# Kernel tuning notes

Hardware: AMD Instinct MI355X
Metric: run time of the kernel (lower is better)

Reference implementation:

```python
import jax, jax.numpy as jnp
import numpy as np
import math

DIM = 1024      # dim == dim_attn (required by value-reshape)
HEAD = 16
KV = 128        # K_v routing slots
HD = DIM // HEAD
N = 50000       # number of nodes


def setup_inputs() -> dict:
    key = jax.random.key(0)
    ks = jax.random.split(key, 8)
    s = lambda fan_in: 1.0 / np.sqrt(fan_in)
    return {
        "x": jax.random.normal(ks[0], (N, DIM), jnp.float32),
        "node_index": jax.random.normal(ks[1], (N, 4), jnp.float32),
        # nn.Linear(dim, dim_attn)
        "Wq": jax.random.normal(ks[2], (DIM, DIM), jnp.float32) * s(DIM),
        "bq": jnp.zeros((DIM,), jnp.float32),
        # nn.Parameter key (K_v, head, head_dim), torch.randn init
        "key_p": jax.random.normal(ks[3], (KV, HEAD, HD), jnp.float32),
        # nn.Linear(dim, dim)
        "Wv": jax.random.normal(ks[4], (DIM, DIM), jnp.float32) * s(DIM),
        "bv": jnp.zeros((DIM,), jnp.float32),
        # gate params, shape (head, 1)
        "alpha": jnp.full((HEAD, 1), math.log(9.0), jnp.float32),
        "beta": jnp.full((HEAD, 1), math.log(0.01), jnp.float32),
        # nn.Linear(4, head*K_v)
        "Wb": jax.random.normal(ks[5], (HEAD * KV, 4), jnp.float32) * s(4),
        "bb": jnp.zeros((HEAD * KV,), jnp.float32),
    }


def _mh_sinkhorn(A, num_iters=3, eps=0.05):
    # A: (N, H, K). Faithful to the per-head torch sinkhorn (Q transposed to
    # (K, N)): row sums are over the node axis, col sums over the slot axis.
    n = A.shape[0]
    k = A.shape[2]
    Q = jnp.exp(A / eps)
    Q = Q / jnp.sum(Q, axis=(0, 2), keepdims=True)          # total-sum norm per head
    for _ in range(num_iters):
        Q = Q / jnp.sum(Q, axis=0, keepdims=True) / k       # rows of Q.T (per slot)
        Q = Q / jnp.sum(Q, axis=2, keepdims=True) / n       # cols of Q.T (per node)
    return Q * n


def reference(x, node_index, Wq, bq, key_p, Wv, bv, alpha, beta, Wb, bb):
    n = x.shape[0]
    q = (x @ Wq.T + bq).reshape(n, HEAD, HD)
    attn = jnp.einsum('nhd,rhd->nhr', q, key_p) / np.float32(np.sqrt(HD))
    bias = (node_index @ Wb.T + bb).reshape(n, HEAD, KV)
    attn = attn + bias                                       # (n, H, K_v)
    xv = (x @ Wv.T + bv).reshape(n, HEAD, HD)
    v = jnp.einsum('nhr,nhd->rhd', jax.nn.sigmoid(attn), xv)  # (K_v, H, D)
    cons = _mh_sinkhorn(jax.nn.softmax(attn, axis=-1))
    v = jnp.einsum('nhr,rhd->nhd', cons, v)
    out = jax.nn.sigmoid(alpha) * xv + jax.nn.sigmoid(beta) * v  # (H,1) broadcasts
    return out.reshape(n, DIM)
```

## Files before the change

### kernel.cpp

```cpp
#include <hip/hip_runtime.h>

#define N_NODES 50000
#define MPAD    50176
#define DIM     1024
#define HEAD    16
#define KV      128
#define HD      64
#define NGRP    98

typedef unsigned short ushort_t;
typedef short short8 __attribute__((ext_vector_type(8)));
typedef float f32x4 __attribute__((ext_vector_type(4)));

__device__ inline unsigned short f2bf(float f){
  union { float f; unsigned u; } v; v.f = f;
  unsigned u = v.u;
  unsigned r = (u + 0x7FFFu + ((u >> 16) & 1u)) >> 16;
  return (unsigned short)r;
}
__device__ inline float bf2f(unsigned short u){
  union { unsigned u; float f; } v; v.u = ((unsigned)u) << 16; return v.f;
}

__device__ inline void gload_lds16(const void* g, void* l){
  __builtin_amdgcn_global_load_lds(
      (const __attribute__((address_space(1))) void*)g,
      (__attribute__((address_space(3))) void*)l, 16, 0, 0);
}

__device__ inline short8 frag64(const ushort_t* lds, int row, int kk, int lane){
  int c  = kk*4 + (lane >> 4);
  int cc = c ^ (row & 7);
  return *(const short8*)(lds + row*64 + cc*8);
}
__device__ inline short8 frag128(const ushort_t* lds, int row, int kk, int lane){
  int c  = kk*4 + (lane >> 4);
  int cc = c ^ (row & 7);
  return *(const short8*)(lds + row*128 + cc*8);
}

__global__ void k_zero(float* p, int n){
  int i = blockIdx.x*256 + threadIdx.x;
  if (i < n) p[i] = 0.f;
}

__global__ void k_prep_x(const float* __restrict__ x, ushort_t* __restrict__ x_bf){
  int idx = blockIdx.x*256 + threadIdx.x;
  int row = idx >> 7, c = idx & 127;
  const float4* s = (const float4*)(x + (size_t)row*1024 + c*8);
  float4 f0 = s[0], f1 = s[1];
  short8 v;
  v[0]=(short)f2bf(f0.x); v[1]=(short)f2bf(f0.y); v[2]=(short)f2bf(f0.z); v[3]=(short)f2bf(f0.w);
  v[4]=(short)f2bf(f1.x); v[5]=(short)f2bf(f1.y); v[6]=(short)f2bf(f1.z); v[7]=(short)f2bf(f1.w);
  int sc = (c & ~7) | ((c ^ row) & 7);
  *(short8*)(x_bf + (size_t)row*1024 + sc*8) = v;
}

__global__ void k_prep_w(const float* __restrict__ Wq, const float* __restrict__ Wv,
                         ushort_t* __restrict__ w_bf){
  int idx = blockIdx.x*256 + threadIdx.x;
  int j = idx >> 10, k = idx & 1023;
  float v = (j < 1024) ? Wq[idx] : Wv[(size_t)(j-1024)*1024 + k];
  int d = k & 63;
  int scol = (k & ~63) | ((((d>>3) ^ (j & 7)) & 7) << 3) | (d & 7);
  w_bf[(size_t)j*1024 + scol] = f2bf(v);
}

__global__ void k_prep_key(const float* __restrict__ key_p, ushort_t* __restrict__ key_bf){
  int idx = blockIdx.x*256 + threadIdx.x;
  int h = idx >> 13, rem = idx & 8191;
  int r = rem >> 6, d = rem & 63;
  float v = key_p[(size_t)(r*HEAD + h)*HD + d];
  int pos = ((((d>>3) ^ (r & 7)) & 7) << 3) | (d & 7);
  key_bf[(size_t)h*8192 + r*64 + pos] = f2bf(v);
}

__global__ void k_vreduce(const float* __restrict__ vp, float* __restrict__ vout){
  int i = blockIdx.x*256 + threadIdx.x;
  float s = 0.f;
  for (int gg = 0; gg < NGRP; ++gg) s += vp[(size_t)gg*131072 + i];
  vout[i] = s;
}

__global__ __launch_bounds__(512) void k_gemm(const ushort_t* __restrict__ x_bf,
    const ushort_t* __restrict__ w_bf, const float* __restrict__ bq,
    const float* __restrict__ bv, ushort_t* __restrict__ q_bf, float* xv_out){
  extern __shared__ char gsm[];
  ushort_t* As = (ushort_t*)gsm;
  ushort_t* Bs = (ushort_t*)(gsm + 65536);
  const int tid = threadIdx.x, lane = tid & 63;
  const int wid = tid >> 6, wr = wid >> 2, wc = wid & 3;
  int b = blockIdx.x;
  int wg = (b & 7)*196 + (b >> 3);
  const int bm0 = (wg >> 3) * 256, bn0 = (wg & 7) * 256;

  f32x4 acc[8][4];
  #pragma unroll
  for (int m=0;m<8;m++)
    #pragma unroll
    for (int n=0;n<4;n++) acc[m][n] = (f32x4){0.f,0.f,0.f,0.f};

  const ushort_t* asrc = x_bf + (size_t)bm0*1024;
  const ushort_t* bsrc = w_bf + (size_t)bn0*1024;

#define STAGE(kt, bi)                                                    \
  { _Pragma("unroll")                                                    \
    for (int it=0; it<4; ++it){                                          \
      int chunk = it*512 + tid;                                          \
      int r = chunk >> 3, c = chunk & 7;                                 \
      gload_lds16(asrc + (size_t)r*1024 + (kt)*64 + c*8,                 \
                  As + (bi)*16384 + chunk*8);                            \
    }                                                                    \
    _Pragma("unroll")                                                    \
    for (int it=0; it<4; ++it){                                          \
      int chunk = it*512 + tid;                                          \
      int r = chunk >> 3, c = chunk & 7;                                 \
      gload_lds16(bsrc + (size_t)r*1024 + (kt)*64 + c*8,                 \
                  Bs + (bi)*16384 + chunk*8);                            \
    }                                                                    \
  }

  STAGE(0, 0);
  STAGE(1, 1);

  for (int kt = 0; kt < 16; ++kt){
    const int cur = kt & 1;
    if (kt == 15) { asm volatile("s_waitcnt vmcnt(0)" ::: "memory"); }
    else          { asm volatile("s_waitcnt vmcnt(8)" ::: "memory"); }
    __builtin_amdgcn_s_barrier();

    const ushort_t* ab  = As + cur*16384;
    const ushort_t* bb_ = Bs + cur*16384;
    #pragma unroll
    for (int kk=0;kk<2;kk++){
      short8 bfr[4];
      #pragma unroll
      for (int n=0;n<4;n++) bfr[n] = frag64(bb_, wc*64 + n*16 + (lane&15), kk, lane);
      #pragma unroll
      for (int m=0;m<8;m++){
        short8 af = frag64(ab, wr*128 + m*16 + (lane&15), kk, lane);
        #pragma unroll
        for (int n=0;n<4;n++)
          acc[m][n] = __builtin_amdgcn_mfma_f32_16x16x32_bf16(af, bfr[n], acc[m][n], 0,0,0);
      }
    }
    __builtin_amdgcn_s_barrier();
    if (kt + 2 < 16) STAGE(kt+2, cur);
  }
#undef STAGE

  const bool isq = bn0 < 1024;
  #pragma unroll
  for (int n=0;n<4;n++){
    int col = bn0 + wc*64 + n*16 + (lane & 15);
    float bias = isq ? bq[col] : bv[col - 1024];
    #pragma unroll
    for (int m=0;m<8;m++){
      #pragma unroll
      for (int j=0;j<4;j++){
        int row = bm0 + wr*128 + m*16 + (lane>>4)*4 + j;
        float val = acc[m][n][j] + bias;
        if (isq){
          int d = col & 63;
          int scol = (col & ~63) | ((((d>>3) ^ (row & 7)) & 7) << 3) | (d & 7);
          q_bf[(size_t)row*1024 + scol] = f2bf(val);
        } else if (row < N_NODES){
          xv_out[(size_t)row*1024 + (col - 1024)] = val;
        }
      }
    }
  }
}

template<int PHASE>
__global__ __launch_bounds__(256) void k_attn(
    const ushort_t* __restrict__ q_bf, const ushort_t* __restrict__ key_bf,
    const float* __restrict__ node_index, const float* __restrict__ Wb,
    const float* __restrict__ bb, const float* __restrict__ colsum_in,
    float* __restrict__ colsum_out, const float* __restrict__ v_fin,
    float* __restrict__ v_part, float* xv_out,
    const float* __restrict__ alpha, const float* __restrict__ beta)
{
  constexpr int QB    = (PHASE == 2) ? 1 : 2;
  constexpr int O_Q   = 0;
  constexpr int O_KEY = O_Q + QB*8192;
  constexpr int O_NI  = O_KEY + 16384;
  constexpr int O_WB  = O_NI + QB*1024;
  constexpr int O_RED = O_WB + 2560;
  constexpr int O_COL = O_RED + 2048;
  constexpr int O_W   = O_COL + 512;
  constexpr int O_X1  = O_W + 512;
  constexpr int O_X2  = O_X1 + 16384;

  extern __shared__ char smem[];
  ushort_t* q_lds   = (ushort_t*)(smem + O_Q);
  ushort_t* key_lds = (ushort_t*)(smem + O_KEY);
  float* ni_lds  = (float*)(smem + O_NI);
  float* wb_lds  = (float*)(smem + O_WB);
  float* red_lds = (float*)(smem + O_RED);
  float* col_acc = (float*)(smem + O_COL);
  float* w_lds   = (float*)(smem + O_W);
  ushort_t* sigT     = (ushort_t*)(smem + O_X1);
  ushort_t* xvT      = (ushort_t*)(smem + O_X2);
  ushort_t* vT       = (ushort_t*)(smem + O_X1);
  ushort_t* cons_lds = (ushort_t*)(smem + O_X2);
  float*    out_lds  = (float*)(smem + O_X2);

  const int tid = threadIdx.x, lane = tid & 63, wid = tid >> 6;
  const int h    = blockIdx.x & 15;
  const int g    = blockIdx.x >> 4;
  const int base = g * 512;
  int NT = (MPAD - base) >> 6; if (NT > 8) NT = 8;

  #pragma unroll
  for (int it = 0; it < 4; ++it){
    int chunk = it*256 + tid;
    gload_lds16(key_bf + (size_t)h*8192 + chunk*8, key_lds + chunk*8);
  }
  #pragma unroll
  for (int it = 0; it < 2; ++it){
    int chunk = it*256 + tid;
    int r = chunk >> 3, c = chunk & 7;
    gload_lds16(q_bf + (size_t)(base + r)*1024 + h*64 + c*8, q_lds + chunk*8);
  }
  { int r = tid >> 2, c = tid & 3;
    ni_lds[tid] = (base + r < N_NODES) ? node_index[(size_t)(base + r)*4 + c] : 0.f; }
  if (tid < 128){
    #pragma unroll
    for (int c=0;c<4;c++) wb_lds[tid*5+c] = Wb[(size_t)(h*128 + tid)*4 + c];
    wb_lds[tid*5+4] = bb[h*128 + tid];
    if (PHASE >= 1) w_lds[tid] = 1.f / (128.f * colsum_in[h*128 + tid]);
    if (PHASE <= 1) col_acc[tid] = 0.f;
  }
  if constexpr (PHASE == 2){
    int r = tid >> 1, dh = (tid & 1)*32;
    #pragma unroll
    for (int i=0;i<32;i++){
      int d = dh + i;
      vT[d*128 + ((r>>3) ^ (d&7))*8 + (r&7)] = f2bf(v_fin[((size_t)r*16 + h)*64 + d]);
    }
  }
  float xvr[16], xvn[16];
  if constexpr (PHASE == 0){
    int d = tid & 63, q4 = tid >> 6;
    #pragma unroll
    for (int i=0;i<16;i++){
      int row = base + q4*16 + i;
      xvr[i] = (row < N_NODES) ? xv_out[(size_t)row*1024 + h*64 + d] : 0.f;
    }
  }
  f32x4 vac[2][4];
  if constexpr (PHASE == 0)
    for (int m=0;m<2;m++) for (int n=0;n<4;n++) vac[m][n] = (f32x4){0.f,0.f,0.f,0.f};

  __syncthreads();

  for (int t = 0; t < NT; ++t){
    const int i0  = base + t*64;
    const int cur = t & 1;
    const ushort_t* qb  = q_lds  + ((QB==2) ? cur*4096 : 0);
    const float*    nib = ni_lds + ((QB==2) ? cur*256  : 0);
    float ni_next = 0.f;

    if constexpr (QB == 2){
      if (t+1 < NT){
        int i1 = i0 + 64;
        #pragma unroll
        for (int it = 0; it < 2; ++it){
          int chunk = it*256 + tid;
          int r = chunk >> 3, c = chunk & 7;
          gload_lds16(q_bf + (size_t)(i1 + r)*1024 + h*64 + c*8,
                      q_lds + (cur^1)*4096 + chunk*8);
        }
        int r = tid >> 2, c = tid & 3;
        ni_next = (i0 + 64 + r < N_NODES) ? node_index[(size_t)(i0+64+r)*4 + c] : 0.f;
      }
    } else {
      if (t+1 < NT){
        int r = tid >> 2, c = tid & 3;
        ni_next = (i0 + 64 + r < N_NODES) ? node_index[(size_t)(i0+64+r)*4 + c] : 0.f;
      }
    }
    if constexpr (PHASE == 0){
      if (t+1 < NT){
        int d = tid & 63, q4 = tid >> 6;
        #pragma unroll
        for (int i=0;i<16;i++){
          int row = i0 + 64 + q4*16 + i;
          xvn[i] = (row < N_NODES) ? xv_out[(size_t)row*1024 + h*64 + d] : 0.f;
        }
      }
    }

    f32x4 acc[2][4];
    for (int m=0;m<2;m++) for (int n=0;n<4;n++) acc[m][n] = (f32x4){0.f,0.f,0.f,0.f};
    #pragma unroll
    for (int kk = 0; kk < 2; ++kk){
      short8 kf[2];
      #pragma unroll
      for (int m=0;m<2;m++) kf[m] = frag64(key_lds, wid*32 + m*16 + (lane&15), kk, lane);
      #pragma unroll
      for (int n=0;n<4;n++){
        short8 qf = frag64(qb, n*16 + (lane&15), kk, lane);
        #pragma unroll
        for (int m=0;m<2;m++)
          acc[m][n] = __builtin_amdgcn_mfma_f32_16x16x32_bf16(kf[m], qf, acc[m][n], 0,0,0);
      }
    }

    float nif[4][4];
    #pragma unroll
    for (int n=0;n<4;n++){
      int nn = n*16 + (lane&15);
      #pragma unroll
      for (int c=0;c<4;c++) nif[n][c] = nib[nn*4+c];
    }
    float a[2][4][4];
    #pragma unroll
    for (int m=0;m<2;m++){
      #pragma unroll
      for (int j=0;j<4;j++){
        int r = wid*32 + m*16 + (lane>>4)*4 + j;
        float w0 = wb_lds[r*5+0], w1 = wb_lds[r*5+1];
        float w2 = wb_lds[r*5+2], w3 = wb_lds[r*5+3], w4 = wb_lds[r*5+4];
        #pragma unroll
        for (int n=0;n<4;n++){
          float b = w4 + w0*nif[n][0] + w1*nif[n][1] + w2*nif[n][2] + w3*nif[n][3];
          a[m][n][j] = acc[m][n][j]*0.125f + b;
        }
      }
    }

    float vmask[4];
    #pragma unroll
    for (int n=0;n<4;n++) vmask[n] = (i0 + n*16 + (lane&15) < N_NODES) ? 1.f : 0.f;

    if constexpr (PHASE == 0){
      #pragma unroll
      for (int m=0;m<2;m++) for (int n=0;n<4;n++) for (int j=0;j<4;j++){
        int r  = wid*32 + m*16 + (lane>>4)*4 + j;
        int nn = n*16 + (lane&15);
        float sg = vmask[n] / (1.f + __expf(-a[m][n][j]));
        sigT[r*64 + ((((nn>>3) ^ (r&7)) & 7) << 3) + (nn&7)] = f2bf(sg);
      }
      { int d = tid & 63, q4 = tid >> 6;
        #pragma unroll
        for (int i=0;i<16;i++){
          int nn = q4*16 + i;
          xvT[d*64 + ((((nn>>3) ^ (d&7)) & 7) << 3) + (nn&7)] = f2bf(xvr[i]);
        }
      }
    }

    float pm[4];
    #pragma unroll
    for (int n=0;n<4;n++){
      float m0 = a[0][n][0];
      #pragma unroll
      for (int m=0;m<2;m++) for (int j=0;j<4;j++) m0 = fmaxf(m0, a[m][n][j]);
      m0 = fmaxf(m0, __shfl_xor(m0, 16));
      m0 = fmaxf(m0, __shfl_xor(m0, 32));
      pm[n] = m0;
    }
    if (lane < 16){
      #pragma unroll
      for (int n=0;n<4;n++) red_lds[wid*64 + n*16 + lane] = pm[n];
    }
    __syncthreads();

    if constexpr (QB == 1){
      if (t+1 < NT){
        int i1 = i0 + 64;
        #pragma unroll
        for (int it = 0; it < 2; ++it){
          int chunk = it*256 + tid;
          int r = chunk >> 3, c = chunk & 7;
          gload_lds16(q_bf + (size_t)(i1 + r)*1024 + h*64 + c*8, q_lds + chunk*8);
        }
        ni_lds[tid] = ni_next;
      }
    }

    float mnn[4], snn[4];
    #pragma unroll
    for (int n=0;n<4;n++){
      int nn = n*16 + (lane&15);
      float m0 = red_lds[nn];
      m0 = fmaxf(m0, red_lds[64+nn]); m0 = fmaxf(m0, red_lds[128+nn]); m0 = fmaxf(m0, red_lds[192+nn]);
      mnn[n] = m0;
    }
    #pragma unroll
    for (int n=0;n<4;n++){
      float s = 0.f;
      #pragma unroll
      for (int m=0;m<2;m++) for (int j=0;j<4;j++){
        float e = __expf(a[m][n][j] - mnn[n]);
        a[m][n][j] = e; s += e;
      }
      s += __shfl_xor(s, 16); s += __shfl_xor(s, 32);
      snn[n] = s;
    }
    if (lane < 16){
      #pragma unroll
      for (int n=0;n<4;n++) red_lds[256 + wid*64 + n*16 + lane] = snn[n];
    }

    if constexpr (PHASE == 0){
      #pragma unroll
      for (int kk=0;kk<2;kk++){
        short8 sa[2];
        #pragma unroll
        for (int m=0;m<2;m++) sa[m] = frag64(sigT, wid*32 + m*16 + (lane&15), kk, lane);
        #pragma unroll
        for (int n=0;n<4;n++){
          short8 xf = frag64(xvT, n*16 + (lane&15), kk, lane);
          #pragma unroll
          for (int m=0;m<2;m++)
            vac[m][n] = __builtin_amdgcn_mfma_f32_16x16x32_bf16(sa[m], xf, vac[m][n], 0,0,0);
        }
      }
    }
    __syncthreads();

    #pragma unroll
    for (int n=0;n<4;n++){
      int nn = n*16 + (lane&15);
      snn[n] = red_lds[256+nn] + red_lds[256+64+nn] + red_lds[256+128+nn] + red_lds[256+192+nn];
    }
    #pragma unroll
    for (int n=0;n<4;n++){
      float inv = 20.f / snn[n];
      #pragma unroll
      for (int m=0;m<2;m++) for (int j=0;j<4;j++)
        a[m][n][j] = __expf(a[m][n][j] * inv);
    }

    float uval[4];
    if constexpr (PHASE >= 1){
      #pragma unroll
      for (int n=0;n<4;n++){
        float s = 0.f;
        #pragma unroll
        for (int m=0;m<2;m++){
          #pragma unroll
          for (int j=0;j<4;j++){
            int r = wid*32 + m*16 + (lane>>4)*4 + j;
            s += a[m][n][j] * w_lds[r];
          }
        }
        s += __shfl_xor(s, 16); s += __shfl_xor(s, 32);
        uval[n] = s;
      }
      if (lane < 16){
        #pragma unroll
        for (int n=0;n<4;n++) red_lds[wid*64 + n*16 + lane] = uval[n];
      }
      __syncthreads();
      #pragma unroll
      for (int n=0;n<4;n++){
        int nn = n*16 + (lane&15);
        float s = red_lds[nn] + red_lds[64+nn] + red_lds[128+nn] + red_lds[192+nn];
        uval[n] = 1.f / (50000.f * s);
      }
    }

    if constexpr (PHASE <= 1){
      float cs[2][4];
      #pragma unroll
      for (int m=0;m<2;m++){
        #pragma unroll
        for (int j=0;j<4;j++){
          float s = 0.f;
          #pragma unroll
          for (int n=0;n<4;n++){
            float tv = a[m][n][j] * vmask[n];
            if (PHASE == 1) tv *= uval[n];
            s += tv;
          }
          s += __shfl_xor(s, 1); s += __shfl_xor(s, 2);
          s += __shfl_xor(s, 4); s += __shfl_xor(s, 8);
          cs[m][j] = s;
        }
      }
      if ((lane & 15) == 0){
        #pragma unroll
        for (int m=0;m<2;m++) for (int j=0;j<4;j++){
          int r = wid*32 + m*16 + (lane>>4)*4 + j;
          col_acc[r] += cs[m][j];
        }
      }
    }

    if constexpr (PHASE == 2){
      #pragma unroll
      for (int m=0;m<2;m++) for (int n=0;n<4;n++) for (int j=0;j<4;j++){
        int r  = wid*32 + m*16 + (lane>>4)*4 + j;
        int nn = n*16 + (lane&15);
        float cv = 50000.f * uval[n] * a[m][n][j] * w_lds[r];
        cons_lds[nn*128 + ((r>>3) ^ (nn&7))*8 + (r&7)] = f2bf(cv);
      }
      __syncthreads();
      f32x4 oac[4];
      for (int n=0;n<4;n++) oac[n] = (f32x4){0.f,0.f,0.f,0.f};
      #pragma unroll
      for (int kk=0;kk<4;kk++){
        short8 va = frag128(vT, wid*16 + (lane&15), kk, lane);
        #pragma unroll
        for (int n=0;n<4;n++){
          short8 cf = frag128(cons_lds, n*16 + (lane&15), kk, lane);
          oac[n] = __builtin_amdgcn_mfma_f32_16x16x32_bf16(va, cf, oac[n], 0,0,0);
        }
      }
      __syncthreads();
      #pragma unroll
      for (int n=0;n<4;n++) for (int j=0;j<4;j++){
        int d  = wid*16 + (lane>>4)*4 + j;
        int nn = n*16 + (lane&15);
        out_lds[nn*68 + d] = oac[n][j];
      }
      __syncthreads();
      float sa = 1.f/(1.f + __expf(-alpha[h]));
      float sb = 1.f/(1.f + __expf(-beta[h]));
      int nn = tid >> 2, d0 = (tid & 3)*16;
      if (i0 + nn < N_NODES){
        #pragma unroll
        for (int gq=0; gq<4; ++gq){
          float4 vf = *(const float4*)(out_lds + nn*68 + d0 + gq*4);
          float4 xf = *(const float4*)(xv_out + (size_t)(i0+nn)*1024 + h*64 + d0 + gq*4);
          float4 o;
          o.x = sa*xf.x + sb*vf.x;
          o.y = sa*xf.y + sb*vf.y;
          o.z = sa*xf.z + sb*vf.z;
          o.w = sa*xf.w + sb*vf.w;
          *(float4*)(xv_out + (size_t)(i0+nn)*1024 + h*64 + d0 + gq*4) = o;
        }
      }
    } else {
      if (t+1 < NT && QB == 2) ni_lds[(cur^1)*256 + tid] = ni_next;
      if constexpr (PHASE == 0){
        if (t+1 < NT){
          #pragma unroll
          for (int i=0;i<16;i++) xvr[i] = xvn[i];
        }
      }
      __syncthreads();
    }
  }

  if constexpr (PHASE == 0){
    float* vdst = v_part + (size_t)g*131072;
    #pragma unroll
    for (int m=0;m<2;m++) for (int n=0;n<4;n++) for (int j=0;j<4;j++){
      int r = wid*32 + m*16 + (lane>>4)*4 + j;
      int d = n*16 + (lane&15);
      vdst[((size_t)r*16 + h)*64 + d] = vac[m][n][j];
    }
  }
  if constexpr (PHASE <= 1){
    if (tid < 128) atomicAdd(&colsum_out[h*128 + tid], col_acc[tid]);
  }
}

extern "C" void kernel_launch(void* const* d_in, const int* in_sizes, int n_in,
                              void* d_out, int out_size, void* d_ws, size_t ws_size,
                              hipStream_t stream){
  const float* x     = (const float*)d_in[0];
  const float* ni    = (const float*)d_in[1];
  const float* Wq    = (const float*)d_in[2];
  const float* bq    = (const float*)d_in[3];
  const float* keyp  = (const float*)d_in[4];
  const float* Wv    = (const float*)d_in[5];
  const float* bv    = (const float*)d_in[6];
  const float* alpha = (const float*)d_in[7];
  const float* beta  = (const float*)d_in[8];
  const float* Wb    = (const float*)d_in[9];
  const float* bb    = (const float*)d_in[10];
  float* out = (float*)d_out;

  char* ws = (char*)d_ws;
  ushort_t* x_bf   = (ushort_t*)(ws);
  float*    v_part = (float*)(ws);
  ushort_t* q_bf   = (ushort_t*)(ws + 102760448);
  ushort_t* w_bf   = (ushort_t*)(ws + 205520896);
  ushort_t* key_bf = (ushort_t*)(ws + 209715200);
  float*    v_fin  = (float*)(ws + 209977344);
  float*    cs     = (float*)(ws + 210501632);

  (void)hipFuncSetAttribute((const void*)k_gemm,
      hipFuncAttributeMaxDynamicSharedMemorySize, 131072);

  k_zero<<<dim3(24), 256, 0, stream>>>(cs, 6144);
  k_zero<<<dim3(352), 256, 0, stream>>>((float*)(x_bf + (size_t)N_NODES*1024), 90112);
  k_prep_x<<<dim3(25000), 256, 0, stream>>>(x, x_bf);
  k_prep_w<<<dim3(2048*1024/256), 256, 0, stream>>>(Wq, Wv, w_bf);
  k_prep_key<<<dim3(HEAD*KV*HD/256), 256, 0, stream>>>(keyp, key_bf);
  k_gemm<<<dim3(1568), 512, 131072, stream>>>(x_bf, w_bf, bq, bv, q_bf, out);

  dim3 ag(NGRP*16);
  k_attn<0><<<ag, 256, 65024, stream>>>(q_bf, key_bf, ni, Wb, bb, nullptr,  cs,      v_fin, v_part, out, alpha, beta);
  k_vreduce<<<dim3(512), 256, 0, stream>>>(v_part, v_fin);
  k_attn<1><<<ag, 256, 40448, stream>>>(q_bf, key_bf, ni, Wb, bb, cs,       cs+2048, v_fin, v_part, out, alpha, beta);
  k_attn<1><<<ag, 256, 40448, stream>>>(q_bf, key_bf, ni, Wb, bb, cs+2048,  cs+4096, v_fin, v_part, out, alpha, beta);
  k_attn<2><<<ag, 256, 65024, stream>>>(q_bf, key_bf, ni, Wb, bb, cs+4096,  nullptr, v_fin, v_part, out, alpha, beta);
}
```

Before: 943.9 us.

## Use 4-stage K=32 pipeline in projection GEMM and stage q stores through LDS

The fused Q/V projection GEMM moves from a double-buffered K=64 tile loop to a four-slot ring of K=32 tiles with three tiles in flight, issuing the next prefetch right after the barrier so global-to-LDS loads overlap compute. The swizzles for x_bf and w_bf change to match the 32-wide tile layout. The q output epilogue now writes bf16 values into an LDS image and then stores coalesced 16-byte rows to global memory instead of scattered 2-byte stores. This adds barriers and a different wait-count schedule, and the prep kernels must stay consistent with the new swizzle.

```diff
diff --git a/kernel.cpp b/kernel.cpp
--- a/kernel.cpp
+++ b/kernel.cpp
@@ -37,6 +37,10 @@
   int c  = kk*4 + (lane >> 4);
   int cc = c ^ (row & 7);
   return *(const short8*)(lds + row*128 + cc*8);
+}
+__device__ inline short8 frag32(const ushort_t* lds, int row, int lane){
+  int p = (lane >> 4) ^ ((row >> 1) & 3);
+  return *(const short8*)(lds + row*32 + p*8);
 }
 
 __global__ void k_zero(float* p, int n){
@@ -52,7 +56,7 @@
   short8 v;
   v[0]=(short)f2bf(f0.x); v[1]=(short)f2bf(f0.y); v[2]=(short)f2bf(f0.z); v[3]=(short)f2bf(f0.w);
   v[4]=(short)f2bf(f1.x); v[5]=(short)f2bf(f1.y); v[6]=(short)f2bf(f1.z); v[7]=(short)f2bf(f1.w);
-  int sc = (c & ~7) | ((c ^ row) & 7);
+  int sc = (c & ~3) | ((c ^ (row >> 1)) & 3);
   *(short8*)(x_bf + (size_t)row*1024 + sc*8) = v;
 }
 
@@ -61,9 +65,9 @@
   int idx = blockIdx.x*256 + threadIdx.x;
   int j = idx >> 10, k = idx & 1023;
   float v = (j < 1024) ? Wq[idx] : Wv[(size_t)(j-1024)*1024 + k];
-  int d = k & 63;
-  int scol = (k & ~63) | ((((d>>3) ^ (j & 7)) & 7) << 3) | (d & 7);
-  w_bf[(size_t)j*1024 + scol] = f2bf(v);
+  int l = k >> 3;
+  int q = (l & ~3) | ((l ^ (j >> 1)) & 3);
+  w_bf[(size_t)j*1024 + q*8 + (k & 7)] = f2bf(v);
 }
 
 __global__ void k_prep_key(const float* __restrict__ key_p, ushort_t* __restrict__ key_bf){
@@ -103,69 +107,92 @@
   const ushort_t* asrc = x_bf + (size_t)bm0*1024;
   const ushort_t* bsrc = w_bf + (size_t)bn0*1024;
 
-#define STAGE(kt, bi)                                                    \
-  { _Pragma("unroll")                                                    \
-    for (int it=0; it<4; ++it){                                          \
-      int chunk = it*512 + tid;                                          \
-      int r = chunk >> 3, c = chunk & 7;                                 \
-      gload_lds16(asrc + (size_t)r*1024 + (kt)*64 + c*8,                 \
-                  As + (bi)*16384 + chunk*8);                            \
-    }                                                                    \
-    _Pragma("unroll")                                                    \
-    for (int it=0; it<4; ++it){                                          \
-      int chunk = it*512 + tid;                                          \
-      int r = chunk >> 3, c = chunk & 7;                                 \
-      gload_lds16(bsrc + (size_t)r*1024 + (kt)*64 + c*8,                 \
-                  Bs + (bi)*16384 + chunk*8);                            \
-    }                                                                    \
+#define STAGE(kt, si)                                                     \
+  { _Pragma("unroll")                                                     \
+    for (int it=0; it<2; ++it){                                           \
+      int chunk = it*512 + tid;                                           \
+      int r = chunk >> 2, c = chunk & 3;                                  \
+      gload_lds16(asrc + (size_t)r*1024 + (kt)*32 + c*8,                  \
+                  As + (si)*8192 + chunk*8);                              \
+      gload_lds16(bsrc + (size_t)r*1024 + (kt)*32 + c*8,                  \
+                  Bs + (si)*8192 + chunk*8);                              \
+    }                                                                     \
   }
 
   STAGE(0, 0);
   STAGE(1, 1);
-
-  for (int kt = 0; kt < 16; ++kt){
-    const int cur = kt & 1;
-    if (kt == 15) { asm volatile("s_waitcnt vmcnt(0)" ::: "memory"); }
-    else          { asm volatile("s_waitcnt vmcnt(8)" ::: "memory"); }
+  STAGE(2, 2);
+
+  for (int t = 0; t < 32; ++t){
+    const int cur = t & 3;
+    if (t < 30)      { asm volatile("s_waitcnt vmcnt(8)" ::: "memory"); }
+    else if (t < 31) { asm volatile("s_waitcnt vmcnt(4)" ::: "memory"); }
+    else             { asm volatile("s_waitcnt vmcnt(0)" ::: "memory"); }
     __builtin_amdgcn_s_barrier();
-
-    const ushort_t* ab  = As + cur*16384;
-    const ushort_t* bb_ = Bs + cur*16384;
-    #pragma unroll
-    for (int kk=0;kk<2;kk++){
-      short8 bfr[4];
-      #pragma unroll
-      for (int n=0;n<4;n++) bfr[n] = frag64(bb_, wc*64 + n*16 + (lane&15), kk, lane);
-      #pragma unroll
-      for (int m=0;m<8;m++){
-        short8 af = frag64(ab, wr*128 + m*16 + (lane&15), kk, lane);
-        #pragma unroll
-        for (int n=0;n<4;n++)
-          acc[m][n] = __builtin_amdgcn_mfma_f32_16x16x32_bf16(af, bfr[n], acc[m][n], 0,0,0);
-      }
+    __builtin_amdgcn_sched_barrier(0);
+    if (t + 3 < 32) STAGE(t+3, (t+3)&3);
+
+    const ushort_t* ab  = As + cur*8192;
+    const ushort_t* bb_ = Bs + cur*8192;
+    short8 bfr[4];
+    #pragma unroll
+    for (int n=0;n<4;n++) bfr[n] = frag32(bb_, wc*64 + n*16 + (lane&15), lane);
+    #pragma unroll
+    for (int m=0;m<8;m++){
+      short8 af = frag32(ab, wr*128 + m*16 + (lane&15), lane);
+      #pragma unroll
+      for (int n=0;n<4;n++)
+        acc[m][n] = __builtin_amdgcn_mfma_f32_16x16x32_bf16(af, bfr[n], acc[m][n], 0,0,0);
     }
     __builtin_amdgcn_s_barrier();
-    if (kt + 2 < 16) STAGE(kt+2, cur);
   }
 #undef STAGE
 
+  __syncthreads();
+
   const bool isq = bn0 < 1024;
+  float biasv[4];
   #pragma unroll
   for (int n=0;n<4;n++){
     int col = bn0 + wc*64 + n*16 + (lane & 15);
-    float bias = isq ? bq[col] : bv[col - 1024];
-    #pragma unroll
-    for (int m=0;m<8;m++){
-      #pragma unroll
-      for (int j=0;j<4;j++){
-        int row = bm0 + wr*128 + m*16 + (lane>>4)*4 + j;
-        float val = acc[m][n][j] + bias;
-        if (isq){
-          int d = col & 63;
-          int scol = (col & ~63) | ((((d>>3) ^ (row & 7)) & 7) << 3) | (d & 7);
-          q_bf[(size_t)row*1024 + scol] = f2bf(val);
-        } else if (row < N_NODES){
-          xv_out[(size_t)row*1024 + (col - 1024)] = val;
+    biasv[n] = isq ? bq[col] : bv[col - 1024];
+  }
+
+  if (isq){
+    ushort_t* img = (ushort_t*)gsm;
+    #pragma unroll
+    for (int n=0;n<4;n++){
+      int lcol = wc*64 + n*16 + (lane & 15);
+      int d = lcol & 63;
+      #pragma unroll
+      for (int m=0;m<8;m++){
+        #pragma unroll
+        for (int j=0;j<4;j++){
+          int lrow = wr*128 + m*16 + (lane>>4)*4 + j;
+          int sc = (lcol & ~63) | ((((d>>3) ^ (lrow & 7)) & 7) << 3) | (d & 7);
+          img[lrow*256 + sc] = f2bf(acc[m][n][j] + biasv[n]);
+        }
+      }
+    }
+    __syncthreads();
+    #pragma unroll
+    for (int it=0; it<16; ++it){
+      int r  = it*16 + (tid >> 5);
+      int ch = tid & 31;
+      short8 v = *(const short8*)(img + r*256 + ch*8);
+      *(short8*)(q_bf + (size_t)(bm0 + r)*1024 + bn0 + ch*8) = v;
+    }
+  } else {
+    #pragma unroll
+    for (int n=0;n<4;n++){
+      int col = bn0 + wc*64 + n*16 + (lane & 15);
+      #pragma unroll
+      for (int m=0;m<8;m++){
+        #pragma unroll
+        for (int j=0;j<4;j++){
+          int row = bm0 + wr*128 + m*16 + (lane>>4)*4 + j;
+          if (row < N_NODES)
+            xv_out[(size_t)row*1024 + (col - 1024)] = acc[m][n][j] + biasv[n];
         }
       }
     }
```

Result: no change. 952.7 us (+0.9%).

## Stage q tile through LDS for coalesced stores and add register-resident sinkhorn kernel

Applied to the files above, without the earlier changes.

The GEMM epilogue for the q half now writes the swizzled bf16 tile into shared memory and then stores whole 16-byte rows to global memory, replacing scattered 2-byte stores. The two middle sinkhorn column-sum passes move to a new k_s1 kernel. Each wave keeps key fragments and bias weights in registers, prefetches the next q fragment, and does softmax and exp in registers with shuffle reductions, with no large LDS allocation. The k_zero launch for the padding region also gets twice as many blocks. The new kernel raises register pressure and uses atomics for the per-head column sums.

```diff
diff --git a/kernel.cpp b/kernel.cpp
--- a/kernel.cpp
+++ b/kernel.cpp
@@ -18,8 +18,8 @@
   unsigned r = (u + 0x7FFFu + ((u >> 16) & 1u)) >> 16;
   return (unsigned short)r;
 }
-__device__ inline float bf2f(unsigned short u){
-  union { unsigned u; float f; } v; v.u = ((unsigned)u) << 16; return v.f;
+__device__ inline float bf2f(unsigned u16){
+  union { unsigned u; float f; } v; v.u = (u16 & 0xFFFFu) << 16; return v.f;
 }
 
 __device__ inline void gload_lds16(const void* g, void* l){
@@ -149,27 +149,192 @@
   }
 #undef STAGE
 
+  __syncthreads();
+
   const bool isq = bn0 < 1024;
+  float biasv[4];
   #pragma unroll
   for (int n=0;n<4;n++){
     int col = bn0 + wc*64 + n*16 + (lane & 15);
-    float bias = isq ? bq[col] : bv[col - 1024];
-    #pragma unroll
-    for (int m=0;m<8;m++){
-      #pragma unroll
-      for (int j=0;j<4;j++){
-        int row = bm0 + wr*128 + m*16 + (lane>>4)*4 + j;
-        float val = acc[m][n][j] + bias;
-        if (isq){
-          int d = col & 63;
-          int scol = (col & ~63) | ((((d>>3) ^ (row & 7)) & 7) << 3) | (d & 7);
-          q_bf[(size_t)row*1024 + scol] = f2bf(val);
-        } else if (row < N_NODES){
-          xv_out[(size_t)row*1024 + (col - 1024)] = val;
-        }
-      }
-    }
-  }
+    biasv[n] = isq ? bq[col] : bv[col - 1024];
+  }
+
+  if (isq){
+    ushort_t* img = (ushort_t*)gsm;
+    #pragma unroll
+    for (int n=0;n<4;n++){
+      int lcol = wc*64 + n*16 + (lane & 15);
+      int d = lcol & 63;
+      #pragma unroll
+      for (int m=0;m<8;m++){
+        #pragma unroll
+        for (int j=0;j<4;j++){
+          int lrow = wr*128 + m*16 + (lane>>4)*4 + j;
+          int sc = (lcol & ~63) | ((((d>>3) ^ (lrow & 7)) & 7) << 3) | (d & 7);
+          img[lrow*256 + sc] = f2bf(acc[m][n][j] + biasv[n]);
+        }
+      }
+    }
+    __syncthreads();
+    #pragma unroll
+    for (int it=0; it<16; ++it){
+      int r  = it*16 + (tid >> 5);
+      int ch = tid & 31;
+      short8 v = *(const short8*)(img + r*256 + ch*8);
+      *(short8*)(q_bf + (size_t)(bm0 + r)*1024 + bn0 + ch*8) = v;
+    }
+  } else {
+    #pragma unroll
+    for (int n=0;n<4;n++){
+      int col = bn0 + wc*64 + n*16 + (lane & 15);
+      #pragma unroll
+      for (int m=0;m<8;m++){
+        #pragma unroll
+        for (int j=0;j<4;j++){
+          int row = bm0 + wr*128 + m*16 + (lane>>4)*4 + j;
+          if (row < N_NODES)
+            xv_out[(size_t)row*1024 + (col - 1024)] = acc[m][n][j] + biasv[n];
+        }
+      }
+    }
+  }
+}
+
+__global__ __launch_bounds__(256) void k_s1(const ushort_t* __restrict__ q_bf,
+    const ushort_t* __restrict__ key_bf, const float* __restrict__ ni,
+    const float* __restrict__ Wb, const float* __restrict__ bb,
+    const float* __restrict__ cs_in, float* __restrict__ cs_out){
+  __shared__ float col_acc[4][128];
+  const int tid = threadIdx.x, lane = tid & 63, wid = tid >> 6;
+  const int h   = blockIdx.x & 15;
+  const int blk = blockIdx.x >> 4;
+  const int gw  = blk*4 + wid;
+  const int cl  = lane & 15, rg = lane >> 4;
+
+  float wbv[8][4], bbr[8], wv[8];
+  #pragma unroll
+  for (int n=0;n<8;n++){
+    int r = h*128 + n*16 + cl;
+    float4 w4 = *(const float4*)(Wb + (size_t)r*4);
+    wbv[n][0]=w4.x; wbv[n][1]=w4.y; wbv[n][2]=w4.z; wbv[n][3]=w4.w;
+    bbr[n] = bb[r];
+    wv[n]  = 1.f/(128.f*cs_in[r]);
+  }
+  short8 kf[8][2];
+  #pragma unroll
+  for (int n=0;n<8;n++)
+    #pragma unroll
+    for (int kk=0;kk<2;kk++){
+      int c = (kk*4+rg) ^ (cl & 7);
+      kf[n][kk] = *(const short8*)(key_bf + (size_t)h*8192 + (n*16+cl)*64 + c*8);
+    }
+
+  float cs_acc[8];
+  #pragma unroll
+  for (int n=0;n<8;n++) cs_acc[n] = 0.f;
+
+  const int g0 = gw*8;
+  short8 qc[2], qn[2];
+  { int row = g0*16 + cl;
+    #pragma unroll
+    for (int kk=0;kk<2;kk++){
+      int c = (kk*4+rg) ^ (row & 7);
+      qc[kk] = *(const short8*)(q_bf + (size_t)row*1024 + h*64 + c*8);
+    } }
+
+  for (int u = 0; u < 8; ++u){
+    const int i0 = (g0+u)*16;
+    if (u+1 < 8){
+      int row = i0 + 16 + cl;
+      #pragma unroll
+      for (int kk=0;kk<2;kk++){
+        int c = (kk*4+rg) ^ (row & 7);
+        qn[kk] = *(const short8*)(q_bf + (size_t)row*1024 + h*64 + c*8);
+      }
+    }
+    float4 ni4[4];
+    #pragma unroll
+    for (int j=0;j<4;j++){
+      int row = i0 + rg*4 + j;
+      if (row < N_NODES) ni4[j] = *(const float4*)(ni + (size_t)row*4);
+      else { ni4[j].x=0.f; ni4[j].y=0.f; ni4[j].z=0.f; ni4[j].w=0.f; }
+    }
+    f32x4 acc[8];
+    #pragma unroll
+    for (int n=0;n<8;n++) acc[n] = (f32x4){0.f,0.f,0.f,0.f};
+    #pragma unroll
+    for (int n=0;n<8;n++){
+      acc[n] = __builtin_amdgcn_mfma_f32_16x16x32_bf16(qc[0], kf[n][0], acc[n], 0,0,0);
+      acc[n] = __builtin_amdgcn_mfma_f32_16x16x32_bf16(qc[1], kf[n][1], acc[n], 0,0,0);
+    }
+    float a[8][4];
+    #pragma unroll
+    for (int n=0;n<8;n++)
+      #pragma unroll
+      for (int j=0;j<4;j++)
+        a[n][j] = acc[n][j]*0.125f
+                + wbv[n][0]*ni4[j].x + wbv[n][1]*ni4[j].y
+                + wbv[n][2]*ni4[j].z + wbv[n][3]*ni4[j].w + bbr[n];
+
+    float mj[4], sj[4];
+    #pragma unroll
+    for (int j=0;j<4;j++){
+      float m0 = a[0][j];
+      #pragma unroll
+      for (int n=1;n<8;n++) m0 = fmaxf(m0, a[n][j]);
+      m0 = fmaxf(m0, __shfl_xor(m0,1));
+      m0 = fmaxf(m0, __shfl_xor(m0,2));
+      m0 = fmaxf(m0, __shfl_xor(m0,4));
+      m0 = fmaxf(m0, __shfl_xor(m0,8));
+      mj[j] = m0;
+    }
+    #pragma unroll
+    for (int j=0;j<4;j++){
+      float s = 0.f;
+      #pragma unroll
+      for (int n=0;n<8;n++){ float e = __expf(a[n][j]-mj[j]); a[n][j]=e; s+=e; }
+      s += __shfl_xor(s,1); s += __shfl_xor(s,2);
+      s += __shfl_xor(s,4); s += __shfl_xor(s,8);
+      sj[j] = s;
+    }
+    #pragma unroll
+    for (int j=0;j<4;j++){
+      float inv = 20.f/sj[j];
+      #pragma unroll
+      for (int n=0;n<8;n++) a[n][j] = __expf(a[n][j]*inv);
+    }
+    float uj[4];
+    #pragma unroll
+    for (int j=0;j<4;j++){
+      float s = 0.f;
+      #pragma unroll
+      for (int n=0;n<8;n++) s += a[n][j]*wv[n];
+      s += __shfl_xor(s,1); s += __shfl_xor(s,2);
+      s += __shfl_xor(s,4); s += __shfl_xor(s,8);
+      int row = i0 + rg*4 + j;
+      uj[j] = (row < N_NODES) ? 1.f/(50000.f*s) : 0.f;
+    }
+    #pragma unroll
+    for (int n=0;n<8;n++)
+      cs_acc[n] += a[n][0]*uj[0] + a[n][1]*uj[1] + a[n][2]*uj[2] + a[n][3]*uj[3];
+
+    qc[0] = qn[0]; qc[1] = qn[1];
+  }
+
+  #pragma unroll
+  for (int n=0;n<8;n++){
+    float v = cs_acc[n];
+    v += __shfl_xor(v,16); v += __shfl_xor(v,32);
+    cs_acc[n] = v;
+  }
+  if (rg == 0){
+    #pragma unroll
+    for (int n=0;n<8;n++) col_acc[wid][n*16+cl] = cs_acc[n];
+  }
+  __syncthreads();
+  if (tid < 128)
+    atomicAdd(&cs_out[h*128+tid],
+      col_acc[0][tid]+col_acc[1][tid]+col_acc[2][tid]+col_acc[3][tid]);
 }
 
 template<int PHASE>
@@ -590,7 +755,7 @@
       hipFuncAttributeMaxDynamicSharedMemorySize, 131072);
 
   k_zero<<<dim3(24), 256, 0, stream>>>(cs, 6144);
-  k_zero<<<dim3(352), 256, 0, stream>>>((float*)(x_bf + (size_t)N_NODES*1024), 90112);
+  k_zero<<<dim3(704), 256, 0, stream>>>((float*)(x_bf + (size_t)N_NODES*1024), 90112);
   k_prep_x<<<dim3(25000), 256, 0, stream>>>(x, x_bf);
   k_prep_w<<<dim3(2048*1024/256), 256, 0, stream>>>(Wq, Wv, w_bf);
   k_prep_key<<<dim3(HEAD*KV*HD/256), 256, 0, stream>>>(keyp, key_bf);
@@ -599,7 +764,7 @@
   dim3 ag(NGRP*16);
   k_attn<0><<<ag, 256, 65024, stream>>>(q_bf, key_bf, ni, Wb, bb, nullptr,  cs,      v_fin, v_part, out, alpha, beta);
   k_vreduce<<<dim3(512), 256, 0, stream>>>(v_part, v_fin);
-  k_attn<1><<<ag, 256, 40448, stream>>>(q_bf, key_bf, ni, Wb, bb, cs,       cs+2048, v_fin, v_part, out, alpha, beta);
-  k_attn<1><<<ag, 256, 40448, stream>>>(q_bf, key_bf, ni, Wb, bb, cs+2048,  cs+4096, v_fin, v_part, out, alpha, beta);
-  k_attn<2><<<ag, 256, 65024, stream>>>(q_bf, key_bf, ni, Wb, bb, cs+4096,  nullptr, v_fin, v_part, out, alpha, beta);
-}
+  k_s1<<<dim3(1568), 256, 0, stream>>>(q_bf, key_bf, ni, Wb, bb, cs,      cs+2048);
+  k_s1<<<dim3(1568), 256, 0, stream>>>(q_bf, key_bf, ni, Wb, bb, cs+2048, cs+4096);
+  k_attn<2><<<ag, 256, 65024, stream>>>(q_bf, key_bf, ni, Wb, bb, cs+4096, nullptr, v_fin, v_part, out, alpha, beta);
+}
```

After: 921.5 us. 2.4% less time.
